# Performance work log

Hardware: AMD Instinct MI355X
Metric: run time of the kernel (lower is better)

## Reference

```python
import jax, jax.numpy as jnp
import numpy as np

N_VARS = 8192
N_CHECKS = 4096
DC = 6          # check degree (edges per check)
DV = 3          # variable degree
N_EDGES = N_CHECKS * DC  # == N_VARS * DV == 24576
NUM_ITERS = 5
BATCH = 2048


def setup_inputs() -> dict:
    key = jax.random.key(0)
    k1, _ = jax.random.split(key)
    channel_llrs = jax.random.normal(k1, (BATCH, N_VARS), dtype=jnp.float32)
    # Regular Tanner graph: edges sorted by check (constant degree DC),
    # variable side is a random permutation with each var appearing DV times.
    H_rows = jnp.asarray(np.repeat(np.arange(N_CHECKS), DC), dtype=jnp.int32)
    rng = np.random.default_rng(0)
    H_cols = jnp.asarray(rng.permutation(np.repeat(np.arange(N_VARS), DV)), dtype=jnp.int32)
    weights = jnp.full((NUM_ITERS, 1), 0.5, dtype=jnp.float32)  # nn.Parameter init
    return {"channel_llrs": channel_llrs, "weights": weights,
            "H_rows": H_rows, "H_cols": H_cols, "n_checks": N_CHECKS}


def _decode(channel_llrs, weights, H_cols, n_checks):
    B, n_vars = channel_llrs.shape
    E = H_cols.shape[0]
    dc = E // n_checks  # constant check degree (edges sorted by check)
    pos = jnp.arange(dc)
    c2v = jnp.zeros((B, E), dtype=channel_llrs.dtype)
    for i in range(weights.shape[0]):
        # variable-node update: sum incoming c2v per variable, exclude self edge
        agg = jnp.zeros((B, n_vars), dtype=channel_llrs.dtype).at[:, H_cols].add(c2v)
        var_llrs = channel_llrs + agg
        v2c = var_llrs[:, H_cols] - c2v                      # [B, E]
        # check-node update (min-sum with self-exclusion), grouped per check
        g = v2c.reshape(B, n_checks, dc)                     # [B, C, dc]
        s = jnp.sign(g)
        prod_s = jnp.prod(s, axis=-1, keepdims=True)
        s_in = jnp.where(s == 0, 1.0, s)                     # torch: sign_in[sign_in==0]=1
        out_sign = prod_s / s_in
        a = jnp.abs(g)
        amin = jnp.min(a, axis=-1, keepdims=True)
        imin = jnp.argmin(a, axis=-1, keepdims=True)
        a2 = jnp.where(pos == imin, jnp.inf, a)
        min2 = jnp.min(a2, axis=-1, keepdims=True)
        min_others = jnp.where(pos == imin, min2, amin)      # min over all-but-self
        c2v = (out_sign * min_others).reshape(B, E) * weights[i]
    final_agg = jnp.zeros((B, n_vars), dtype=channel_llrs.dtype).at[:, H_cols].add(c2v)
    return channel_llrs + final_agg


def reference(channel_llrs, weights, H_rows, H_cols, n_checks):
    # H_rows == repeat(arange(n_checks), dc) by construction; grouping is done
    # via the [n_checks, dc] reshape (same partition as the original per-check loop).
    return _decode(channel_llrs, weights, H_cols, n_checks)
```

## Files before the change

### kernel.cpp

```cpp
#include <hip/hip_runtime.h>
#include <stdint.h>

#define NV    8192
#define NC    4096
#define DC    6
#define DV    3
#define NE    24576
#define NITER 5
#define BATCH 2048


__global__ void build_v2e(const int* __restrict__ cols, int* __restrict__ cnt,
                          unsigned short* __restrict__ v2e_tmp) {
  int e = blockIdx.x * blockDim.x + threadIdx.x;
  if (e >= NE) return;
  int v = cols[e];
  int s = atomicAdd(&cnt[v], 1);
  v2e_tmp[v * DV + s] = (unsigned short)e;
}

__global__ void invert_slots(const unsigned short* __restrict__ v2e_tmp,
                             unsigned short* __restrict__ slotp16) {
  int v = blockIdx.x * blockDim.x + threadIdx.x;
  if (v >= NV) return;
  int a = v2e_tmp[v * 3 + 0];
  int b = v2e_tmp[v * 3 + 1];
  int c = v2e_tmp[v * 3 + 2];
  int t;
  if (a > b) { t = a; a = b; b = t; }
  if (b > c) { t = b; b = c; c = t; }
  if (a > b) { t = a; a = b; b = t; }
  int e3[3] = {a, b, c};
#pragma unroll
  for (int k = 0; k < 3; ++k) {
    int e = e3[k];
    int cc = e / DC;
    int j = e - cc * DC;
    slotp16[((j >> 1) * NC + cc) * 2 + (j & 1)] = (unsigned short)(k * NV + v);
  }
}


__global__ __launch_bounds__(1024) void decode_kernel(
    const float* __restrict__ ch, const float* __restrict__ wts,
    const unsigned int* __restrict__ slotp, float* __restrict__ out) {
  __shared__ float s_msg[NE];

  const int tid = threadIdx.x;
  const int b = blockIdx.x;
  const float* chrow = ch + (size_t)b * NV;

  float chreg[8];
#pragma unroll
  for (int r = 0; r < 8; ++r) chreg[r] = chrow[tid + r * 1024];

  float w[NITER];
#pragma unroll
  for (int i = 0; i < NITER; ++i) w[i] = wts[i];

  int idx[4][6];
#pragma unroll
  for (int r = 0; r < 4; ++r) {
    int c = tid + r * 1024;
    unsigned int p0 = slotp[c];
    unsigned int p1 = slotp[NC + c];
    unsigned int p2 = slotp[2 * NC + c];
    idx[r][0] = (int)(p0 & 0xFFFFu); idx[r][1] = (int)(p0 >> 16);
    idx[r][2] = (int)(p1 & 0xFFFFu); idx[r][3] = (int)(p1 >> 16);
    idx[r][4] = (int)(p2 & 0xFFFFu); idx[r][5] = (int)(p2 >> 16);
  }

#pragma unroll
  for (int r = 0; r < 8; ++r) {
    int v = tid + r * 1024;
    float vl = chreg[r];
    s_msg[v] = vl;
    s_msg[NV + v] = vl;
    s_msg[2 * NV + v] = vl;
  }
  __syncthreads();

  for (int it = 0; it < NITER; ++it) {
    const float wi = w[it];

#pragma unroll
    for (int r = 0; r < 4; ++r) {
      unsigned int u[6];
      float m1 = INFINITY, m2 = INFINITY;
      unsigned int xs = 0u;
#pragma unroll
      for (int j = 0; j < 6; ++j) {
        float t = s_msg[idx[r][j]];
        unsigned int uu = __float_as_uint(t);
        u[j] = uu;
        xs ^= uu;
        float a = fabsf(t);
        m2 = fminf(m2, fmaxf(m1, a));
        m1 = fminf(m1, a);
      }
      const bool anyz = (m1 == 0.0f);
      const float m1w = m1 * wi;
      const float m2w = m2 * wi;
#pragma unroll
      for (int j = 0; j < 6; ++j) {
        float a = __uint_as_float(u[j] & 0x7FFFFFFFu);
        float mag = (a == m1) ? m2w : m1w;
        unsigned int s = (xs ^ u[j]) & 0x80000000u;
        float o = __uint_as_float(__float_as_uint(mag) ^ s);
        if (anyz) o = 0.0f;
        s_msg[idx[r][j]] = o;
      }
    }
    __syncthreads();

    if (it < NITER - 1) {
#pragma unroll
      for (int r = 0; r < 8; ++r) {
        int v = tid + r * 1024;
        float c0 = s_msg[v];
        float c1 = s_msg[NV + v];
        float c2 = s_msg[2 * NV + v];
        float vl = chreg[r] + ((c0 + c1) + c2);
        s_msg[v] = vl - c0;
        s_msg[NV + v] = vl - c1;
        s_msg[2 * NV + v] = vl - c2;
      }
      __syncthreads();
    }
  }

  float* orow = out + (size_t)b * NV;
#pragma unroll
  for (int r = 0; r < 8; ++r) {
    int v = tid + r * 1024;
    float c0 = s_msg[v];
    float c1 = s_msg[NV + v];
    float c2 = s_msg[2 * NV + v];
    orow[v] = chreg[r] + ((c0 + c1) + c2);
  }
}


extern "C" void kernel_launch(void* const* d_in, const int* in_sizes, int n_in,
                              void* d_out, int out_size, void* d_ws, size_t ws_size,
                              hipStream_t stream) {
  (void)in_sizes; (void)n_in; (void)out_size; (void)ws_size;

  const float* ch   = (const float*)d_in[0];
  const float* wts  = (const float*)d_in[1];
  const int*  Hcols = (const int*)d_in[3];
  float* out = (float*)d_out;

  char* ws = (char*)d_ws;
  int*            cnt     = (int*)(ws + 0);
  unsigned short* v2e_tmp = (unsigned short*)(ws + 32768);
  unsigned int*   slotp   = (unsigned int*)(ws + 81920);

  hipMemsetAsync(cnt, 0, NV * sizeof(int), stream);
  build_v2e<<<(NE + 255) / 256, 256, 0, stream>>>(Hcols, cnt, v2e_tmp);
  invert_slots<<<(NV + 255) / 256, 256, 0, stream>>>(v2e_tmp, (unsigned short*)slotp);

  decode_kernel<<<BATCH, 1024, 0, stream>>>(ch, wts, slotp, out);
}
```

Baseline: 167.3 us.

## Reorder per-check edge slots to avoid LDS bank conflicts; vectorize variable pass

```diff
diff --git a/kernel.cpp b/kernel.cpp
--- a/kernel.cpp
+++ b/kernel.cpp
@@ -20,7 +20,7 @@
 }
 
 __global__ void invert_slots(const unsigned short* __restrict__ v2e_tmp,
-                             unsigned short* __restrict__ slotp16) {
+                             unsigned short* __restrict__ cslot) {
   int v = blockIdx.x * blockDim.x + threadIdx.x;
   if (v >= NV) return;
   int a = v2e_tmp[v * 3 + 0];
@@ -30,14 +30,54 @@
   if (a > b) { t = a; a = b; b = t; }
   if (b > c) { t = b; b = c; c = t; }
   if (a > b) { t = a; a = b; b = t; }
-  int e3[3] = {a, b, c};
-#pragma unroll
-  for (int k = 0; k < 3; ++k) {
-    int e = e3[k];
-    int cc = e / DC;
-    int j = e - cc * DC;
-    slotp16[((j >> 1) * NC + cc) * 2 + (j & 1)] = (unsigned short)(k * NV + v);
-  }
+  cslot[a] = (unsigned short)(0 * NV + v);
+  cslot[b] = (unsigned short)(1 * NV + v);
+  cslot[c] = (unsigned short)(2 * NV + v);
+}
+
+
+__global__ __launch_bounds__(64) void greedy_schedule(
+    const unsigned short* __restrict__ cslot, unsigned int* __restrict__ slotp) {
+  __shared__ unsigned short sl[64][6];
+  __shared__ unsigned short pm[64][6];
+  __shared__ int cnt[32];
+
+  const int l = threadIdx.x;
+  const int c = blockIdx.x * 64 + l;
+
+  const unsigned int* cs32 = (const unsigned int*)cslot;
+  unsigned int a0 = cs32[c * 3 + 0];
+  unsigned int a1 = cs32[c * 3 + 1];
+  unsigned int a2 = cs32[c * 3 + 2];
+  sl[l][0] = (unsigned short)(a0 & 0xffffu); sl[l][1] = (unsigned short)(a0 >> 16);
+  sl[l][2] = (unsigned short)(a1 & 0xffffu); sl[l][3] = (unsigned short)(a1 >> 16);
+  sl[l][4] = (unsigned short)(a2 & 0xffffu); sl[l][5] = (unsigned short)(a2 >> 16);
+
+  unsigned int used = 0;
+  for (int j = 0; j < 6; ++j) {
+    if (l < 32) cnt[l] = 0;
+    __syncthreads();
+    int placed = -1;
+    for (int k = 0; k < 6; ++k) {
+      if (placed >= 0) break;
+      if (used & (1u << k)) continue;
+      int bk = sl[l][k] & 31;
+      int old = atomicAdd(&cnt[bk], 1);
+      if (old < 2) placed = k;
+      else atomicSub(&cnt[bk], 1);
+    }
+    if (placed < 0) {
+      for (int k = 0; k < 6; ++k)
+        if (!(used & (1u << k))) { placed = k; break; }
+    }
+    used |= (1u << placed);
+    pm[l][j] = sl[l][placed];
+    __syncthreads();
+  }
+
+  slotp[0 * NC + c] = (unsigned int)pm[l][0] | ((unsigned int)pm[l][1] << 16);
+  slotp[1 * NC + c] = (unsigned int)pm[l][2] | ((unsigned int)pm[l][3] << 16);
+  slotp[2 * NC + c] = (unsigned int)pm[l][4] | ((unsigned int)pm[l][5] << 16);
 }
 
 
@@ -49,10 +89,11 @@
   const int tid = threadIdx.x;
   const int b = blockIdx.x;
   const float* chrow = ch + (size_t)b * NV;
-
-  float chreg[8];
-#pragma unroll
-  for (int r = 0; r < 8; ++r) chreg[r] = chrow[tid + r * 1024];
+  const float4* ch4 = (const float4*)chrow;
+
+  float4 chreg[2];
+  chreg[0] = ch4[tid];
+  chreg[1] = ch4[1024 + tid];
 
   float w[NITER];
 #pragma unroll
@@ -70,13 +111,15 @@
     idx[r][4] = (int)(p2 & 0xFFFFu); idx[r][5] = (int)(p2 >> 16);
   }
 
-#pragma unroll
-  for (int r = 0; r < 8; ++r) {
-    int v = tid + r * 1024;
-    float vl = chreg[r];
-    s_msg[v] = vl;
-    s_msg[NV + v] = vl;
-    s_msg[2 * NV + v] = vl;
+  float4* m0 = (float4*)&s_msg[0];
+  float4* m1 = (float4*)&s_msg[NV];
+  float4* m2 = (float4*)&s_msg[2 * NV];
+
+#pragma unroll
+  for (int p = 0; p < 2; ++p) {
+    int i4 = p * 1024 + tid;
+    float4 v = chreg[p];
+    m0[i4] = v; m1[i4] = v; m2[i4] = v;
   }
   __syncthreads();
 
@@ -86,7 +129,7 @@
 #pragma unroll
     for (int r = 0; r < 4; ++r) {
       unsigned int u[6];
-      float m1 = INFINITY, m2 = INFINITY;
+      float m1v = INFINITY, m2v = INFINITY;
       unsigned int xs = 0u;
 #pragma unroll
       for (int j = 0; j < 6; ++j) {
@@ -95,16 +138,16 @@
         u[j] = uu;
         xs ^= uu;
         float a = fabsf(t);
-        m2 = fminf(m2, fmaxf(m1, a));
-        m1 = fminf(m1, a);
+        m2v = fminf(m2v, fmaxf(m1v, a));
+        m1v = fminf(m1v, a);
       }
-      const bool anyz = (m1 == 0.0f);
-      const float m1w = m1 * wi;
-      const float m2w = m2 * wi;
+      const bool anyz = (m1v == 0.0f);
+      const float m1w = m1v * wi;
+      const float m2w = m2v * wi;
 #pragma unroll
       for (int j = 0; j < 6; ++j) {
         float a = __uint_as_float(u[j] & 0x7FFFFFFFu);
-        float mag = (a == m1) ? m2w : m1w;
+        float mag = (a == m1v) ? m2w : m1w;
         unsigned int s = (xs ^ u[j]) & 0x80000000u;
         float o = __uint_as_float(__float_as_uint(mag) ^ s);
         if (anyz) o = 0.0f;
@@ -115,28 +158,36 @@
 
     if (it < NITER - 1) {
 #pragma unroll
-      for (int r = 0; r < 8; ++r) {
-        int v = tid + r * 1024;
-        float c0 = s_msg[v];
-        float c1 = s_msg[NV + v];
-        float c2 = s_msg[2 * NV + v];
-        float vl = chreg[r] + ((c0 + c1) + c2);
-        s_msg[v] = vl - c0;
-        s_msg[NV + v] = vl - c1;
-        s_msg[2 * NV + v] = vl - c2;
+      for (int p = 0; p < 2; ++p) {
+        int i4 = p * 1024 + tid;
+        float4 c0 = m0[i4], c1 = m1[i4], c2 = m2[i4];
+        float4 cr = chreg[p];
+        float4 vl;
+        vl.x = cr.x + ((c0.x + c1.x) + c2.x);
+        vl.y = cr.y + ((c0.y + c1.y) + c2.y);
+        vl.z = cr.z + ((c0.z + c1.z) + c2.z);
+        vl.w = cr.w + ((c0.w + c1.w) + c2.w);
+        float4 o0 = {vl.x - c0.x, vl.y - c0.y, vl.z - c0.z, vl.w - c0.w};
+        float4 o1 = {vl.x - c1.x, vl.y - c1.y, vl.z - c1.z, vl.w - c1.w};
+        float4 o2 = {vl.x - c2.x, vl.y - c2.y, vl.z - c2.z, vl.w - c2.w};
+        m0[i4] = o0; m1[i4] = o1; m2[i4] = o2;
       }
       __syncthreads();
     }
   }
 
-  float* orow = out + (size_t)b * NV;
-#pragma unroll
-  for (int r = 0; r < 8; ++r) {
-    int v = tid + r * 1024;
-    float c0 = s_msg[v];
-    float c1 = s_msg[NV + v];
-    float c2 = s_msg[2 * NV + v];
-    orow[v] = chreg[r] + ((c0 + c1) + c2);
+  float4* orow4 = (float4*)(out + (size_t)b * NV);
+#pragma unroll
+  for (int p = 0; p < 2; ++p) {
+    int i4 = p * 1024 + tid;
+    float4 c0 = m0[i4], c1 = m1[i4], c2 = m2[i4];
+    float4 cr = chreg[p];
+    float4 o;
+    o.x = cr.x + ((c0.x + c1.x) + c2.x);
+    o.y = cr.y + ((c0.y + c1.y) + c2.y);
+    o.z = cr.z + ((c0.z + c1.z) + c2.z);
+    o.w = cr.w + ((c0.w + c1.w) + c2.w);
+    orow4[i4] = o;
   }
 }
 
@@ -154,11 +205,13 @@
   char* ws = (char*)d_ws;
   int*            cnt     = (int*)(ws + 0);
   unsigned short* v2e_tmp = (unsigned short*)(ws + 32768);
-  unsigned int*   slotp   = (unsigned int*)(ws + 81920);
+  unsigned short* cslot   = (unsigned short*)(ws + 81920);
+  unsigned int*   slotp   = (unsigned int*)(ws + 131072);
 
   hipMemsetAsync(cnt, 0, NV * sizeof(int), stream);
   build_v2e<<<(NE + 255) / 256, 256, 0, stream>>>(Hcols, cnt, v2e_tmp);
-  invert_slots<<<(NV + 255) / 256, 256, 0, stream>>>(v2e_tmp, (unsigned short*)slotp);
+  invert_slots<<<(NV + 255) / 256, 256, 0, stream>>>(v2e_tmp, cslot);
+  greedy_schedule<<<NC / 64, 64, 0, stream>>>(cslot, slotp);
 
   decode_kernel<<<BATCH, 1024, 0, stream>>>(ch, wts, slotp, out);
 }
```

Measured after the change: 150.6 us. -10.0%, faster.
